# Kernel tuning notes

Hardware: AMD Instinct MI355X
Metric: run time of the kernel (lower is better)

The kernel has to match this reference:

```python
import jax, jax.numpy as jnp
import numpy as np

EMB = 64          # emb_size
LG = 64           # lg_msg_dim
NDB = 16          # num_dist_basis
NCB = 16          # num_cos_basis
NCLS = 40
NLAYERS = 2
NJK = NLAYERS + 2  # jumping-knowledge sequence length
HID = (NJK * EMB) // 2  # PyG JK-LSTM hidden size = 128


def setup_inputs() -> dict:
    key = jax.random.key(0)
    ks = jax.random.split(key, 24)
    N, Eg, Elg, F = 50000, 800000, 800000, 128
    s = 0.05
    inp = {
        "x": jax.random.normal(ks[0], (N, F), jnp.float32),
        "edge_index_g": jax.random.randint(ks[1], (2, Eg), 0, N, jnp.int32),
        "edge_attr_g": jax.random.uniform(ks[2], (Eg, NDB), jnp.float32),
        "edge_index_lg": jax.random.randint(ks[3], (2, Elg), 0, Eg, jnp.int32),
        "edge_attr_lg": jax.random.uniform(ks[4], (Elg, NCB), jnp.float32),
        # parameters (nn.Linear convention: W is [out, in])
        "W_feat": jax.random.normal(ks[5], (EMB, F), jnp.float32) * s,
        "W_msg": jax.random.normal(ks[6], (LG, 2 * EMB + NDB), jnp.float32) * s,
        "W_lg2g": jax.random.normal(ks[7], (EMB, LG), jnp.float32) * s,
        "b_lg2g": jax.random.normal(ks[8], (EMB,), jnp.float32) * s,
        "W_msg_layers": jax.random.normal(ks[9], (NLAYERS, LG, 2 * LG + NCB), jnp.float32) * s,
        # bidirectional LSTM params (PyTorch gate order i,f,g,o)
        "Wih_f": jax.random.normal(ks[10], (4 * HID, EMB), jnp.float32) * s,
        "Whh_f": jax.random.normal(ks[11], (4 * HID, HID), jnp.float32) * s,
        "bih_f": jax.random.normal(ks[12], (4 * HID,), jnp.float32) * s,
        "bhh_f": jax.random.normal(ks[13], (4 * HID,), jnp.float32) * s,
        "Wih_b": jax.random.normal(ks[14], (4 * HID, EMB), jnp.float32) * s,
        "Whh_b": jax.random.normal(ks[15], (4 * HID, HID), jnp.float32) * s,
        "bih_b": jax.random.normal(ks[16], (4 * HID,), jnp.float32) * s,
        "bhh_b": jax.random.normal(ks[17], (4 * HID,), jnp.float32) * s,
        "W_att": jax.random.normal(ks[18], (1, 2 * HID), jnp.float32) * s,
        "b_att": jax.random.normal(ks[19], (1,), jnp.float32) * s,
        "W_out": jax.random.normal(ks[20], (NCLS, EMB), jnp.float32) * s,
    }
    return inp


def _lstm(x_seq, Wih, Whh, bih, bhh, reverse):
    # x_seq: [N, L, C] -> hs: [N, L, H]
    N = x_seq.shape[0]
    H = Whh.shape[1]
    b = bih + bhh

    def step(carry, x_t):
        h, c = carry
        gates = x_t @ Wih.T + h @ Whh.T + b
        i, f, g, o = jnp.split(gates, 4, axis=-1)
        c = jax.nn.sigmoid(f) * c + jax.nn.sigmoid(i) * jnp.tanh(g)
        h = jax.nn.sigmoid(o) * jnp.tanh(c)
        return (h, c), h

    xs = jnp.swapaxes(x_seq, 0, 1)  # [L, N, C]
    init = (jnp.zeros((N, H), x_seq.dtype), jnp.zeros((N, H), x_seq.dtype))
    _, hs = jax.lax.scan(step, init, xs, reverse=reverse)
    return jnp.swapaxes(hs, 0, 1)


def reference(x, edge_index_g, edge_attr_g, edge_index_lg, edge_attr_lg,
              W_feat, W_msg, W_lg2g, b_lg2g, W_msg_layers,
              Wih_f, Whh_f, bih_f, bhh_f, Wih_b, Whh_b, bih_b, bhh_b,
              W_att, b_att, W_out):
    N = x.shape[0]
    Eg = edge_attr_g.shape[0]
    seg = jax.ops.segment_sum

    # node embedding (eval mode: dropout is identity)
    node_emb = jax.nn.relu(x @ W_feat.T)  # [N, EMB]

    # initial linegraph node features: gather endpoints -> concat -> linear -> relu
    m1 = node_emb[edge_index_g[0]]  # [Eg, EMB]
    m2 = node_emb[edge_index_g[1]]
    msg_emb = jax.nn.relu(jnp.concatenate([m1, m2, edge_attr_g], -1) @ W_msg.T)  # [Eg, LG]

    node_embs = [node_emb]
    msg_red = msg_emb @ W_lg2g.T + b_lg2g
    node_embs.append(seg(msg_red, edge_index_g[1], num_segments=N))

    # message-passing layers on the linegraph
    for l in range(W_msg_layers.shape[0]):
        s = msg_emb[edge_index_lg[0]]
        d = msg_emb[edge_index_lg[1]]
        m = jax.nn.relu(jnp.concatenate([s, d, edge_attr_lg], -1) @ W_msg_layers[l].T)
        msg_emb = seg(m, edge_index_lg[1], num_segments=Eg)  # scatter_add over linegraph
        incoming = seg(msg_emb, edge_index_g[1], num_segments=N)
        node_embs.append(incoming @ W_lg2g.T + b_lg2g)

    # JumpingKnowledge ('lstm'): bidirectional LSTM -> attention -> weighted sum
    x_jk = jnp.stack(node_embs, axis=1)  # [N, NJK, EMB]
    h_f = _lstm(x_jk, Wih_f, Whh_f, bih_f, bhh_f, reverse=False)
    h_b = _lstm(x_jk, Wih_b, Whh_b, bih_b, bhh_b, reverse=True)
    h = jnp.concatenate([h_f, h_b], -1)  # [N, NJK, 2*HID]
    alpha = jax.nn.softmax((h @ W_att.T + b_att)[..., 0], axis=-1)  # [N, NJK]
    final_emb = jnp.sum(x_jk * alpha[..., None], axis=1)  # [N, EMB]

    out = final_emb @ W_out.T
    return jax.nn.log_softmax(out, axis=-1)
```

## Files before the change

### kernel.cpp

```cpp
#include <hip/hip_runtime.h>

typedef unsigned short u16;
typedef unsigned int u32;
typedef __attribute__((ext_vector_type(8))) short bf16x8;
typedef __attribute__((ext_vector_type(4))) float f32x4;

#define MFMA(a, b, c) __builtin_amdgcn_mfma_f32_16x16x32_bf16(a, b, c, 0, 0, 0)

__device__ __forceinline__ u16 f2bf(float x) {
    union { float f; u32 u; } v; v.f = x;
    u32 r = (v.u + 0x7FFFu + ((v.u >> 16) & 1u)) >> 16;
    return (u16)r;
}
__device__ __forceinline__ float bf2f(u16 b) {
    union { u32 u; float f; } v; v.u = ((u32)b) << 16;
    return v.f;
}
__device__ __forceinline__ void casAddPair(u32* w, float lo, float hi) {
    u32 old = *w, assumed;
    do {
        assumed = old;
        u32 des = (u32)f2bf(bf2f((u16)(assumed & 0xFFFFu)) + lo) |
                  ((u32)f2bf(bf2f((u16)(assumed >> 16)) + hi) << 16);
        if (des == assumed) break;
        old = atomicCAS(w, assumed, des);
    } while (old != assumed);
}

__global__ __launch_bounds__(256) void prep_w(
    const float* __restrict__ Whh_f, const float* __restrict__ Whh_b,
    const float* __restrict__ Wih_f, const float* __restrict__ Wih_b,
    const float* __restrict__ bih_f, const float* __restrict__ bhh_f,
    const float* __restrict__ bih_b, const float* __restrict__ bhh_b,
    u16* __restrict__ WhhB, u16* __restrict__ WihB, float* __restrict__ BS)
{
    int i = blockIdx.x * 256 + threadIdx.x;
    if (i < 131072) {
        int d = i >> 16, r = i & 65535;
        WhhB[i] = f2bf(d ? Whh_b[r] : Whh_f[r]);
    } else if (i < 196608) {
        int i2 = i - 131072; int d = i2 >> 15, r = i2 & 32767;
        WihB[i2] = f2bf(d ? Wih_b[r] : Wih_f[r]);
    } else if (i < 197632) {
        int i3 = i - 196608; int d = i3 >> 9, g = i3 & 511;
        BS[i3] = d ? (bih_b[g] + bhh_b[g]) : (bih_f[g] + bhh_f[g]);
    }
}

__global__ __launch_bounds__(256) void count_kernel(const int* __restrict__ dst,
                                                    u32* __restrict__ cnt, long E)
{
    long i = (long)blockIdx.x * 256 + threadIdx.x;
    if (i < E) atomicAdd(&cnt[dst[i]], 1u);
}

__global__ __launch_bounds__(256) void scan1(const u32* __restrict__ a,
                                             u32* __restrict__ part, int n)
{
    __shared__ u32 ts[256];
    int b = blockIdx.x, t = threadIdx.x;
    long i0 = (long)b * 1024 + t * 4;
    u32 s = 0;
#pragma unroll
    for (int k = 0; k < 4; ++k) { long i = i0 + k; if (i < n) s += a[i]; }
    ts[t] = s; __syncthreads();
    for (int off = 1; off < 256; off <<= 1) {
        u32 x = (t >= off) ? ts[t - off] : 0u;
        __syncthreads(); ts[t] += x; __syncthreads();
    }
    if (t == 255) part[b] = ts[255];
}

__global__ __launch_bounds__(1024) void scan2(u32* __restrict__ part, int nb,
                                              u32* __restrict__ total_out)
{
    __shared__ u32 ts[1024];
    int t = threadIdx.x;
    u32 v = (t < nb) ? part[t] : 0u;
    ts[t] = v; __syncthreads();
    for (int off = 1; off < 1024; off <<= 1) {
        u32 x = (t >= off) ? ts[t - off] : 0u;
        __syncthreads(); ts[t] += x; __syncthreads();
    }
    if (t < nb) part[t] = ts[t] - v;
    if (t == 1023 && total_out) *total_out = ts[1023];
}

__global__ __launch_bounds__(256) void scan3(u32* __restrict__ a,
                                             const u32* __restrict__ part, int n)
{
    __shared__ u32 ts[256];
    int b = blockIdx.x, t = threadIdx.x;
    long i0 = (long)b * 1024 + t * 4;
    u32 v[4]; u32 s = 0;
#pragma unroll
    for (int k = 0; k < 4; ++k) { long i = i0 + k; v[k] = (i < n) ? a[i] : 0u; s += v[k]; }
    ts[t] = s; __syncthreads();
    for (int off = 1; off < 256; off <<= 1) {
        u32 x = (t >= off) ? ts[t - off] : 0u;
        __syncthreads(); ts[t] += x; __syncthreads();
    }
    u32 run = part[b] + ts[t] - s;
#pragma unroll
    for (int k = 0; k < 4; ++k) {
        long i = i0 + k;
        if (i < n) { u32 x = v[k]; a[i] = run; run += x; }
    }
}

__global__ __launch_bounds__(256) void fill_kernel(const int* __restrict__ dst,
                                                   u32* __restrict__ off,
                                                   int* __restrict__ list, long E)
{
    long i = (long)blockIdx.x * 256 + threadIdx.x;
    if (i < E) {
        u32 pos = atomicAdd(&off[dst[i]], 1u);
        list[pos] = (int)i;
    }
}

__global__ __launch_bounds__(256) void zero_fill(const u32* __restrict__ offc,
                                                 u16* __restrict__ outb, long NB)
{
    long idx = (long)blockIdx.x * 256 + threadIdx.x;
    long n = idx >> 3; int q = (int)(idx & 7);
    if (n >= NB) return;
    u32 s = n ? offc[n - 1] : 0u;
    u32 e = offc[n];
    bool need = (s == e) || ((s >> 7) != ((e - 1) >> 7));
    if (need) *(uint4*)(outb + n * 64 + q * 8) = make_uint4(0, 0, 0, 0);
}

template <int K, bool RELU, bool INBF16>
__global__ __launch_bounds__(256) void rowgemm(
    const void* __restrict__ in, const float* __restrict__ W,
    const float* __restrict__ bias, const float* __restrict__ bias_scale,
    u16* __restrict__ outb, int M)
{
    constexpr int KP = K + 8;
    __shared__ u16 inS[64 * KP];
    __shared__ u16 WS[64 * KP];
    int t = threadIdx.x;
    long rb = (long)blockIdx.x * 64;
    for (int i = t; i < 64 * K; i += 256) {
        int c = i / K, k = i - c * K;
        WS[c * KP + k] = f2bf(W[i]);
    }
    if (INBF16) {
        const u16* inb = (const u16*)in;
        for (int i = t; i < 64 * K / 8; i += 256) {
            int r = i / (K / 8), q = i - r * (K / 8);
            long gr = rb + r;
            uint4 v = make_uint4(0, 0, 0, 0);
            if (gr < M) v = *(const uint4*)&inb[gr * (long)K + q * 8];
            *(uint4*)&inS[r * KP + q * 8] = v;
        }
    } else {
        const float* inf = (const float*)in;
        for (int i = t; i < 64 * K; i += 256) {
            int r = i / K, k = i - r * K;
            long gr = rb + r;
            inS[r * KP + k] = (gr < M) ? f2bf(inf[gr * (long)K + k]) : (u16)0;
        }
    }
    __syncthreads();
    int l = t & 63, w = t >> 6, lr = l & 15, lq = l >> 4;
    f32x4 acc[4];
#pragma unroll
    for (int i = 0; i < 4; ++i) acc[i] = (f32x4){0.f, 0.f, 0.f, 0.f};
#pragma unroll
    for (int kc = 0; kc < K; kc += 32) {
        bf16x8 a = *(const bf16x8*)&inS[(w * 16 + lr) * KP + kc + lq * 8];
#pragma unroll
        for (int ct = 0; ct < 4; ++ct) {
            bf16x8 b = *(const bf16x8*)&WS[(ct * 16 + lr) * KP + kc + lq * 8];
            acc[ct] = MFMA(a, b, acc[ct]);
        }
    }
#pragma unroll
    for (int ct = 0; ct < 4; ++ct)
#pragma unroll
        for (int r = 0; r < 4; ++r) {
            long gr = rb + w * 16 + lq * 4 + r;
            if (gr < M) {
                int c = ct * 16 + lr;
                float v = acc[ct][r];
                if (bias) v += bias[c] * (bias_scale ? bias_scale[gr] : 1.f);
                if (RELU) v = fmaxf(v, 0.f);
                outb[gr * 64 + c] = f2bf(v);
            }
        }
}

__global__ __launch_bounds__(512, 4) void edge_msg_init2(
    const u16* __restrict__ feat, const int* __restrict__ ei,
    const float* __restrict__ attr, const float* __restrict__ W,
    u16* __restrict__ outb, long E)
{
    __shared__ u16 WS[64 * 168];
    __shared__ u16 eds[128 * 64];
    int t = threadIdx.x;
    long eb = (long)blockIdx.x * 128;
    for (int i = t; i < 64 * 144; i += 512) {
        int c = i / 144, k = i - c * 144;
        WS[c * 168 + k] = f2bf(W[i]);
    }
    for (int i = t; i < 64 * 24; i += 512) {
        int c = i / 24, k = 144 + (i - c * 24);
        WS[c * 168 + k] = 0;
    }
    int w = t >> 6, l = t & 63, lr = l & 15, lq = l >> 4;
    long e = eb + w * 16 + lr;
    long ec = (e < E) ? e : (E - 1);
    int src = ei[ec], dst = ei[E + ec];
    bf16x8 A[5];
    {
        const uint4* sp = (const uint4*)(feat + (long)src * 64);
        const uint4* dp = (const uint4*)(feat + (long)dst * 64);
        *(uint4*)&A[0] = sp[lq];
        *(uint4*)&A[1] = sp[4 + lq];
        *(uint4*)&A[2] = dp[lq];
        *(uint4*)&A[3] = dp[4 + lq];
        uint4 pv = make_uint4(0, 0, 0, 0);
        if (lq < 2) {
            const float4* ap = (const float4*)(attr + ec * 16) + lq * 2;
            float4 b0 = ap[0], b1 = ap[1];
            pv.x = (u32)f2bf(b0.x) | ((u32)f2bf(b0.y) << 16);
            pv.y = (u32)f2bf(b0.z) | ((u32)f2bf(b0.w) << 16);
            pv.z = (u32)f2bf(b1.x) | ((u32)f2bf(b1.y) << 16);
            pv.w = (u32)f2bf(b1.z) | ((u32)f2bf(b1.w) << 16);
        }
        *(uint4*)&A[4] = pv;
    }
    __syncthreads();
    f32x4 acc[4];
#pragma unroll
    for (int ct = 0; ct < 4; ++ct) acc[ct] = (f32x4){0.f, 0.f, 0.f, 0.f};
#pragma unroll
    for (int kc = 0; kc < 5; ++kc) {
#pragma unroll
        for (int ct = 0; ct < 4; ++ct) {
            bf16x8 b = *(const bf16x8*)&WS[(ct * 16 + lr) * 168 + kc * 32 + lq * 8];
            acc[ct] = MFMA(A[kc], b, acc[ct]);
        }
    }
#pragma unroll
    for (int ct = 0; ct < 4; ++ct)
#pragma unroll
        for (int r = 0; r < 4; ++r) {
            int row = w * 16 + lq * 4 + r;
            int col = ct * 16 + lr;
            eds[row * 64 + col] = f2bf(fmaxf(acc[ct][r], 0.f));
        }
    __syncthreads();
    for (int j = t; j < 1024; j += 512) {
        int le = j >> 3, q = j & 7;
        long e2 = eb + le;
        if (e2 < E)
            *(uint4*)(outb + e2 * 64 + q * 8) = *(const uint4*)&eds[le * 64 + q * 8];
    }
}

__global__ __launch_bounds__(512, 4) void edge_msg_lg2(
    const u16* __restrict__ feat, const int* __restrict__ ei,
    const float* __restrict__ attr, const float* __restrict__ W,
    const int* __restrict__ list, u16* __restrict__ outb, long E)
{
    __shared__ u16 WS[64 * 168];
    __shared__ u16 eds[128 * 64];
    __shared__ int dstS[128];
    __shared__ int idS[128];
    __shared__ int srcS[128];
    __shared__ int dprevS, dnextS;
    int t = threadIdx.x;
    long pb = (long)blockIdx.x * 128;
    for (int i = t; i < 64 * 144; i += 512) {
        int c = i / 144, k = i - c * 144;
        WS[c * 168 + k] = f2bf(W[i]);
    }
    for (int i = t; i < 64 * 24; i += 512) {
        int c = i / 24, k = 144 + (i - c * 24);
        WS[c * 168 + k] = 0;
    }
    if (t < 128) {
        long p = pb + t;
        int id = (p < E) ? list[p] : -1;
        idS[t] = id;
        srcS[t] = (id >= 0) ? ei[id] : 0;
        dstS[t] = (id >= 0) ? ei[E + id] : -1;
    } else if (t == 128) {
        dprevS = (pb > 0) ? ei[E + list[pb - 1]] : -2;
    } else if (t == 129) {
        dnextS = (pb + 128 < E) ? ei[E + list[pb + 128]] : -2;
    }
    __syncthreads();
    int w = t >> 6, l = t & 63, lr = l & 15, lq = l >> 4;
    int el = w * 16 + lr;
    int id = idS[el];
    long idc = (id >= 0) ? (long)id : 0;
    int src = srcS[el];
    int dst = (dstS[el] >= 0) ? dstS[el] : 0;
    bf16x8 A[5];
    {
        const uint4* sp = (const uint4*)(feat + (long)src * 64);
        const uint4* dp = (const uint4*)(feat + (long)dst * 64);
        *(uint4*)&A[0] = sp[lq];
        *(uint4*)&A[1] = sp[4 + lq];
        *(uint4*)&A[2] = dp[lq];
        *(uint4*)&A[3] = dp[4 + lq];
        uint4 pv = make_uint4(0, 0, 0, 0);
        if (lq < 2) {
            const float4* ap = (const float4*)(attr + idc * 16) + lq * 2;
            float4 b0 = ap[0], b1 = ap[1];
            pv.x = (u32)f2bf(b0.x) | ((u32)f2bf(b0.y) << 16);
            pv.y = (u32)f2bf(b0.z) | ((u32)f2bf(b0.w) << 16);
            pv.z = (u32)f2bf(b1.x) | ((u32)f2bf(b1.y) << 16);
            pv.w = (u32)f2bf(b1.z) | ((u32)f2bf(b1.w) << 16);
        }
        *(uint4*)&A[4] = pv;
    }
    f32x4 acc[4];
#pragma unroll
    for (int ct = 0; ct < 4; ++ct) acc[ct] = (f32x4){0.f, 0.f, 0.f, 0.f};
#pragma unroll
    for (int kc = 0; kc < 5; ++kc) {
#pragma unroll
        for (int ct = 0; ct < 4; ++ct) {
            bf16x8 b = *(const bf16x8*)&WS[(ct * 16 + lr) * 168 + kc * 32 + lq * 8];
            acc[ct] = MFMA(A[kc], b, acc[ct]);
        }
    }
#pragma unroll
    for (int ct = 0; ct < 4; ++ct)
#pragma unroll
        for (int r = 0; r < 4; ++r) {
            int row = w * 16 + lq * 4 + r;
            int col = ct * 16 + lr;
            eds[row * 64 + col] = f2bf(fmaxf(acc[ct][r], 0.f));
        }
    __syncthreads();
    for (int j = t; j < 4096; j += 512) {
        int le = j >> 5, wd = j & 31;
        int d = dstS[le];
        if (d < 0) continue;
        if (le > 0 && dstS[le - 1] == d) continue;
        float lo = 0.f, hi = 0.f;
        int le2 = le;
        do {
            u32 pair = *(const u32*)&eds[le2 * 64 + wd * 2];
            lo += bf2f((u16)(pair & 0xFFFFu));
            hi += bf2f((u16)(pair >> 16));
            ++le2;
        } while (le2 < 128 && dstS[le2] == d);
        bool bprev = (le == 0 && dprevS == d);
        bool bnext = (le2 == 128 && dnextS == d);
        u32* dw = (u32*)(outb + (long)d * 64 + wd * 2);
        if (bprev || bnext) {
            casAddPair(dw, lo, hi);
        } else {
            *dw = (u32)f2bf(lo) | ((u32)f2bf(hi) << 16);
        }
    }
}

__global__ __launch_bounds__(256) void gather_g(
    const u16* __restrict__ m, const int* __restrict__ list,
    const u32* __restrict__ offc, u16* __restrict__ aggB,
    float* __restrict__ degOut, int N)
{
    int t = threadIdx.x;
    int hw = t >> 5, c = t & 31;
    long n = (long)blockIdx.x * 8 + hw;
    if (n >= N) return;
    u32 start = n ? offc[n - 1] : 0u;
    u32 end = offc[n];
    float s0 = 0.f, s1 = 0.f;
    for (u32 i = start; i < end; ++i) {
        int e = list[i];
        u32 pair = *(const u32*)&m[(long)e * 64 + c * 2];
        s0 += bf2f((u16)(pair & 0xFFFFu));
        s1 += bf2f((u16)(pair >> 16));
    }
    *(u32*)&aggB[n * 64 + c * 2] = (u32)f2bf(s0) | ((u32)f2bf(s1) << 16);
    if (degOut && c == 0) degOut[n] = (float)(end - start);
}

__global__ __launch_bounds__(512, 2) void lstm3(
    const u16* __restrict__ jkB, const u16* __restrict__ WhhB,
    const u16* __restrict__ WihB, const float* __restrict__ BS,
    const float* __restrict__ Watt, float* __restrict__ scores,
    int N, int ntiles)
{
    __shared__ u16 hS[64 * 136];
    __shared__ u16 xS[64 * 72];
    __shared__ float WattS[128];
    __shared__ float part[64 * 8];
    int t = threadIdx.x;
    int dir = blockIdx.y;
    int w = t >> 6, l = t & 63, lr = l & 15, lq = l >> 4;
    const u16* WhhD = WhhB + (long)dir * 65536;
    const u16* WihD = WihB + (long)dir * 32768;
    int grow = w * 16 + lr;
    bf16x8 Wh[4][4], Wi[4][2];
    float bs[4];
#pragma unroll
    for (int ty = 0; ty < 4; ++ty) {
        int g = ty * 128 + grow;
#pragma unroll
        for (int kc = 0; kc < 4; ++kc)
            Wh[ty][kc] = *(const bf16x8*)&WhhD[g * 128 + kc * 32 + lq * 8];
#pragma unroll
        for (int kc = 0; kc < 2; ++kc)
            Wi[ty][kc] = *(const bf16x8*)&WihD[g * 64 + kc * 32 + lq * 8];
        bs[ty] = BS[dir * 512 + g];
    }
    if (t < 128) WattS[t] = Watt[dir * 128 + t];
    float* scOut = scores + (long)dir * N * 4;

    for (int tile = blockIdx.x; tile < ntiles; tile += gridDim.x) {
        long n0 = (long)tile * 64;
        __syncthreads();
        for (int i = t; i < 64 * 136; i += 512) hS[i] = 0;
        float creg[4][4] = {};
#pragma unroll 1
        for (int s = 0; s < 4; ++s) {
            int tt = dir ? (3 - s) : s;
            {
                int n = t >> 3, j = t & 7;
                long gn = n0 + n;
                uint4 v = make_uint4(0, 0, 0, 0);
                if (gn < N) v = *(const uint4*)&jkB[((long)tt * N + gn) * 64 + j * 8];
                *(uint4*)&xS[n * 72 + j * 8] = v;
            }
            __syncthreads();
            f32x4 acc[4][4];
#pragma unroll
            for (int ty = 0; ty < 4; ++ty)
#pragma unroll
                for (int nt = 0; nt < 4; ++nt) {
                    float b0 = bs[ty];
                    acc[ty][nt] = (f32x4){b0, b0, b0, b0};
                }
#pragma unroll
            for (int kc = 0; kc < 4; ++kc) {
                bf16x8 a[4];
#pragma unroll
                for (int nt = 0; nt < 4; ++nt)
                    a[nt] = *(const bf16x8*)&hS[(nt * 16 + lr) * 136 + kc * 32 + lq * 8];
#pragma unroll
                for (int ty = 0; ty < 4; ++ty)
#pragma unroll
                    for (int nt = 0; nt < 4; ++nt)
                        acc[ty][nt] = MFMA(a[nt], Wh[ty][kc], acc[ty][nt]);
            }
#pragma unroll
            for (int kc = 0; kc < 2; ++kc) {
                bf16x8 a[4];
#pragma unroll
                for (int nt = 0; nt < 4; ++nt)
                    a[nt] = *(const bf16x8*)&xS[(nt * 16 + lr) * 72 + kc * 32 + lq * 8];
#pragma unroll
                for (int ty = 0; ty < 4; ++ty)
#pragma unroll
                    for (int nt = 0; nt < 4; ++nt)
                        acc[ty][nt] = MFMA(a[nt], Wi[ty][kc], acc[ty][nt]);
            }
            __syncthreads();
#pragma unroll
            for (int nt = 0; nt < 4; ++nt)
#pragma unroll
                for (int r = 0; r < 4; ++r) {
                    float iv = acc[0][nt][r], fv = acc[1][nt][r];
                    float gv = acc[2][nt][r], ov = acc[3][nt][r];
                    float c = creg[nt][r];
                    float si = 1.f / (1.f + __expf(-iv));
                    float sf = 1.f / (1.f + __expf(-fv));
                    float tg = 2.f / (1.f + __expf(-2.f * gv)) - 1.f;
                    c = sf * c + si * tg;
                    float so = 1.f / (1.f + __expf(-ov));
                    float th = 2.f / (1.f + __expf(-2.f * c)) - 1.f;
                    creg[nt][r] = c;
                    int node = nt * 16 + lq * 4 + r;
                    hS[node * 136 + grow] = f2bf(so * th);
                }
            __syncthreads();
            {
                int n = t & 63, ck = t >> 6;
                float sum = 0.f;
#pragma unroll
                for (int j = 0; j < 16; ++j)
                    sum += bf2f(hS[n * 136 + ck * 16 + j]) * WattS[ck * 16 + j];
                part[n * 8 + ck] = sum;
            }
            __syncthreads();
            if (t < 64) {
                long gn = n0 + t;
                if (gn < N) {
                    float v = 0.f;
#pragma unroll
                    for (int j = 0; j < 8; ++j) v += part[t * 8 + j];
                    scOut[gn * 4 + tt] = v;
                }
            }
        }
    }
}

__global__ __launch_bounds__(256) void final_kernel(
    const u16* __restrict__ jkB, const float* __restrict__ scores,
    const float* __restrict__ Wout, float* __restrict__ out, int N)
{
    __shared__ float feS[4][64];
    int t = threadIdx.x, l = t & 63, w = t >> 6;
    long n = (long)blockIdx.x * 4 + w;
    bool ok = (n < N);
    long nn = ok ? n : (long)(N - 1);
    float sc[4];
#pragma unroll
    for (int tt = 0; tt < 4; ++tt)
        sc[tt] = scores[nn * 4 + tt] + scores[(long)N * 4 + nn * 4 + tt];
    float m = fmaxf(fmaxf(sc[0], sc[1]), fmaxf(sc[2], sc[3]));
    float e0 = __expf(sc[0] - m), e1 = __expf(sc[1] - m);
    float e2 = __expf(sc[2] - m), e3 = __expf(sc[3] - m);
    float den = e0 + e1 + e2 + e3;
    float a0 = e0 / den, a1 = e1 / den, a2 = e2 / den, a3 = e3 / den;
    float fe = a0 * bf2f(jkB[nn * 64 + l]) + a1 * bf2f(jkB[((long)N + nn) * 64 + l]) +
               a2 * bf2f(jkB[((long)2 * N + nn) * 64 + l]) +
               a3 * bf2f(jkB[((long)3 * N + nn) * 64 + l]);
    feS[w][l] = fe;
    __syncthreads();
    float logit = 0.f;
    if (l < 40)
        for (int c = 0; c < 64; ++c) logit += feS[w][c] * Wout[l * 64 + c];
    float v = (l < 40) ? logit : -1e30f;
    for (int off = 32; off; off >>= 1) v = fmaxf(v, __shfl_xor(v, off));
    float ex = (l < 40) ? __expf(logit - v) : 0.f;
    for (int off = 32; off; off >>= 1) ex += __shfl_xor(ex, off);
    if (ok && l < 40) out[n * 40 + l] = logit - v - __logf(ex);
}

extern "C" void kernel_launch(void* const* d_in, const int* in_sizes, int n_in,
                              void* d_out, int out_size, void* d_ws, size_t ws_size,
                              hipStream_t stream)
{
    const float* x        = (const float*)d_in[0];
    const int*   eig      = (const int*)d_in[1];
    const float* eag      = (const float*)d_in[2];
    const int*   eilg     = (const int*)d_in[3];
    const float* ealg     = (const float*)d_in[4];
    const float* W_feat   = (const float*)d_in[5];
    const float* W_msg    = (const float*)d_in[6];
    const float* W_lg2g   = (const float*)d_in[7];
    const float* b_lg2g   = (const float*)d_in[8];
    const float* W_msg_l  = (const float*)d_in[9];
    const float* Wih_f    = (const float*)d_in[10];
    const float* Whh_f    = (const float*)d_in[11];
    const float* bih_f    = (const float*)d_in[12];
    const float* bhh_f    = (const float*)d_in[13];
    const float* Wih_b    = (const float*)d_in[14];
    const float* Whh_b    = (const float*)d_in[15];
    const float* bih_b    = (const float*)d_in[16];
    const float* bhh_b    = (const float*)d_in[17];
    const float* W_att    = (const float*)d_in[18];
    const float* W_out    = (const float*)d_in[20];

    int  N   = in_sizes[0] / 128;
    long Eg  = in_sizes[1] / 2;
    long Elg = in_sizes[3] / 2;

    char* wp = (char*)d_ws;
    auto alloc = [&](size_t bytes) -> char* {
        char* p = wp; wp += (bytes + 255) & ~(size_t)255; return p;
    };
    u16*   jkB    = (u16*)  alloc((size_t)4 * N * 64 * 2);
    u16*   mA     = (u16*)  alloc((size_t)Eg * 64 * 2);
    u16*   mB     = (u16*)  alloc((size_t)Eg * 64 * 2);
    u16*   aggB   = (u16*)  alloc((size_t)N * 64 * 2);
    float* deg    = (float*)alloc((size_t)N * 4);
    float* scores = (float*)alloc((size_t)2 * N * 4 * 4);
    u16*   WhhB   = (u16*)  alloc((size_t)2 * 65536 * 2);
    u16*   WihB   = (u16*)  alloc((size_t)2 * 32768 * 2);
    float* BS     = (float*)alloc((size_t)2 * 512 * 4);
    u32*   off_g  = (u32*)  alloc((size_t)(N + 1) * 4);
    int*   list_g = (int*)  alloc((size_t)Eg * 4);
    u32*   off_lg = (u32*)  alloc((size_t)(Eg + 1) * 4);
    int*   list_lg= (int*)  alloc((size_t)Elg * 4);
    u32*   part   = (u32*)  alloc((size_t)1024 * 4);

    prep_w<<<772, 256, 0, stream>>>(Whh_f, Whh_b, Wih_f, Wih_b,
                                    bih_f, bhh_f, bih_b, bhh_b, WhhB, WihB, BS);
    hipMemsetAsync(off_g, 0, (size_t)(N + 1) * 4, stream);
    count_kernel<<<(int)((Eg + 255) / 256), 256, 0, stream>>>(eig + Eg, off_g, Eg);
    {
        int nb = (N + 1023) / 1024;
        scan1<<<nb, 256, 0, stream>>>(off_g, part, N);
        scan2<<<1, 1024, 0, stream>>>(part, nb, off_g + N);
        scan3<<<nb, 256, 0, stream>>>(off_g, part, N);
    }
    fill_kernel<<<(int)((Eg + 255) / 256), 256, 0, stream>>>(eig + Eg, off_g, list_g, Eg);
    hipMemsetAsync(off_lg, 0, (size_t)(Eg + 1) * 4, stream);
    count_kernel<<<(int)((Elg + 255) / 256), 256, 0, stream>>>(eilg + Elg, off_lg, Elg);
    {
        int nb = (int)((Eg + 1023) / 1024);
        scan1<<<nb, 256, 0, stream>>>(off_lg, part, (int)Eg);
        scan2<<<1, 1024, 0, stream>>>(part, nb, off_lg + Eg);
        scan3<<<nb, 256, 0, stream>>>(off_lg, part, (int)Eg);
    }
    fill_kernel<<<(int)((Elg + 255) / 256), 256, 0, stream>>>(eilg + Elg, off_lg, list_lg, Elg);

    rowgemm<128, true, false><<<(N + 63) / 64, 256, 0, stream>>>(
        x, W_feat, nullptr, nullptr, jkB, N);
    edge_msg_init2<<<(int)((Eg + 127) / 128), 512, 0, stream>>>(
        jkB, eig, eag, W_msg, mA, Eg);
    gather_g<<<(N + 7) / 8, 256, 0, stream>>>(mA, list_g, off_g, aggB, deg, N);
    rowgemm<64, false, true><<<(N + 63) / 64, 256, 0, stream>>>(
        aggB, W_lg2g, b_lg2g, deg, jkB + (size_t)N * 64, N);
    zero_fill<<<(int)((Eg * 8 + 255) / 256), 256, 0, stream>>>(off_lg, mB, Eg);
    edge_msg_lg2<<<(int)((Elg + 127) / 128), 512, 0, stream>>>(
        mA, eilg, ealg, W_msg_l, list_lg, mB, Elg);
    gather_g<<<(N + 7) / 8, 256, 0, stream>>>(mB, list_g, off_g, aggB, nullptr, N);
    rowgemm<64, false, true><<<(N + 63) / 64, 256, 0, stream>>>(
        aggB, W_lg2g, b_lg2g, nullptr, jkB + (size_t)2 * N * 64, N);
    zero_fill<<<(int)((Eg * 8 + 255) / 256), 256, 0, stream>>>(off_lg, mA, Eg);
    edge_msg_lg2<<<(int)((Elg + 127) / 128), 512, 0, stream>>>(
        mB, eilg, ealg, W_msg_l + 64 * 144, list_lg, mA, Elg);
    gather_g<<<(N + 7) / 8, 256, 0, stream>>>(mA, list_g, off_g, aggB, nullptr, N);
    rowgemm<64, false, true><<<(N + 63) / 64, 256, 0, stream>>>(
        aggB, W_lg2g, b_lg2g, nullptr, jkB + (size_t)3 * N * 64, N);
    {
        int ntiles = (N + 63) / 64;
        lstm3<<<dim3(512, 2), 512, 0, stream>>>(
            jkB, WhhB, WihB, BS, W_att, scores, N, ntiles);
    }
    final_kernel<<<(N + 3) / 4, 256, 0, stream>>>(
        jkB, scores, W_out, (float*)d_out, N);
}
```

Before: 1.136 ms.

## Restructure JK-LSTM kernel: one tile per block, preload inputs, fused attention reduce

The LSTM kernel now launches one block per 64-node tile instead of a persistent grid loop, and preloads all four timestep inputs into shared memory up front. The log2(e) scaling is folded into the weights and biases at prep time so the gates use raw exp2 and rcp intrinsics. The MFMA operands are swapped so each lane holds four consecutive gate rows, which lets the attention dot product be done in registers with shuffles. The first step's recurrent GEMM is skipped because h is zero, and several barriers are removed. The trade-off is more shared memory per block, reloading weights in every block, and slightly lower precision in the approximate transcendentals.

```diff
diff --git a/kernel.cpp b/kernel.cpp
--- a/kernel.cpp
+++ b/kernel.cpp
@@ -34,16 +34,20 @@
     const float* __restrict__ bih_b, const float* __restrict__ bhh_b,
     u16* __restrict__ WhhB, u16* __restrict__ WihB, float* __restrict__ BS)
 {
+    const float L2E = 1.4426950408889634f;
     int i = blockIdx.x * 256 + threadIdx.x;
     if (i < 131072) {
         int d = i >> 16, r = i & 65535;
-        WhhB[i] = f2bf(d ? Whh_b[r] : Whh_f[r]);
+        float s = (((r >> 14) & 3) == 2) ? 2.f * L2E : L2E;
+        WhhB[i] = f2bf(s * (d ? Whh_b[r] : Whh_f[r]));
     } else if (i < 196608) {
         int i2 = i - 131072; int d = i2 >> 15, r = i2 & 32767;
-        WihB[i2] = f2bf(d ? Wih_b[r] : Wih_f[r]);
+        float s = (((r >> 13) & 3) == 2) ? 2.f * L2E : L2E;
+        WihB[i2] = f2bf(s * (d ? Wih_b[r] : Wih_f[r]));
     } else if (i < 197632) {
         int i3 = i - 196608; int d = i3 >> 9, g = i3 & 511;
-        BS[i3] = d ? (bih_b[g] + bhh_b[g]) : (bih_f[g] + bhh_f[g]);
+        float s = (((g >> 7) & 3) == 2) ? 2.f * L2E : L2E;
+        BS[i3] = s * (d ? (bih_b[g] + bhh_b[g]) : (bih_f[g] + bhh_f[g]));
     }
 }
 
@@ -389,58 +393,60 @@
     const u16* __restrict__ jkB, const u16* __restrict__ WhhB,
     const u16* __restrict__ WihB, const float* __restrict__ BS,
     const float* __restrict__ Watt, float* __restrict__ scores,
-    int N, int ntiles)
+    int N)
 {
     __shared__ u16 hS[64 * 136];
-    __shared__ u16 xS[64 * 72];
-    __shared__ float WattS[128];
-    __shared__ float part[64 * 8];
+    __shared__ u16 xS[4][64 * 72];
+    __shared__ float part[4 * 64 * 8];
     int t = threadIdx.x;
     int dir = blockIdx.y;
     int w = t >> 6, l = t & 63, lr = l & 15, lq = l >> 4;
     const u16* WhhD = WhhB + (long)dir * 65536;
     const u16* WihD = WihB + (long)dir * 32768;
-    int grow = w * 16 + lr;
+    long n0 = (long)blockIdx.x * 64;
+
+    {
+        int n = t >> 3, j = t & 7;
+        long gn = n0 + n;
+#pragma unroll
+        for (int k = 0; k < 4; ++k) {
+            uint4 v = make_uint4(0, 0, 0, 0);
+            if (gn < N) v = *(const uint4*)&jkB[((long)k * N + gn) * 64 + j * 8];
+            *(uint4*)&xS[k][n * 72 + j * 8] = v;
+        }
+    }
+
+    int grow0 = w * 16 + lq * 4;
     bf16x8 Wh[4][4], Wi[4][2];
-    float bs[4];
+    float4 b4[4];
 #pragma unroll
     for (int ty = 0; ty < 4; ++ty) {
-        int g = ty * 128 + grow;
+        int g = ty * 128 + w * 16 + lr;
 #pragma unroll
         for (int kc = 0; kc < 4; ++kc)
             Wh[ty][kc] = *(const bf16x8*)&WhhD[g * 128 + kc * 32 + lq * 8];
 #pragma unroll
         for (int kc = 0; kc < 2; ++kc)
             Wi[ty][kc] = *(const bf16x8*)&WihD[g * 64 + kc * 32 + lq * 8];
-        bs[ty] = BS[dir * 512 + g];
-    }
-    if (t < 128) WattS[t] = Watt[dir * 128 + t];
+        b4[ty] = *(const float4*)&BS[dir * 512 + ty * 128 + grow0];
+    }
+    float4 Wa4 = *(const float4*)&Watt[dir * 128 + grow0];
     float* scOut = scores + (long)dir * N * 4;
 
-    for (int tile = blockIdx.x; tile < ntiles; tile += gridDim.x) {
-        long n0 = (long)tile * 64;
-        __syncthreads();
-        for (int i = t; i < 64 * 136; i += 512) hS[i] = 0;
-        float creg[4][4] = {};
+    float creg[4][4] = {};
+    __syncthreads();
+
 #pragma unroll 1
-        for (int s = 0; s < 4; ++s) {
-            int tt = dir ? (3 - s) : s;
-            {
-                int n = t >> 3, j = t & 7;
-                long gn = n0 + n;
-                uint4 v = make_uint4(0, 0, 0, 0);
-                if (gn < N) v = *(const uint4*)&jkB[((long)tt * N + gn) * 64 + j * 8];
-                *(uint4*)&xS[n * 72 + j * 8] = v;
-            }
-            __syncthreads();
-            f32x4 acc[4][4];
-#pragma unroll
-            for (int ty = 0; ty < 4; ++ty)
-#pragma unroll
-                for (int nt = 0; nt < 4; ++nt) {
-                    float b0 = bs[ty];
-                    acc[ty][nt] = (f32x4){b0, b0, b0, b0};
-                }
+    for (int s = 0; s < 4; ++s) {
+        int tt = dir ? (3 - s) : s;
+        f32x4 acc[4][4];
+#pragma unroll
+        for (int ty = 0; ty < 4; ++ty) {
+            f32x4 bv = {b4[ty].x, b4[ty].y, b4[ty].z, b4[ty].w};
+#pragma unroll
+            for (int nt = 0; nt < 4; ++nt) acc[ty][nt] = bv;
+        }
+        if (s) {
 #pragma unroll
             for (int kc = 0; kc < 4; ++kc) {
                 bf16x8 a[4];
@@ -451,57 +457,60 @@
                 for (int ty = 0; ty < 4; ++ty)
 #pragma unroll
                     for (int nt = 0; nt < 4; ++nt)
-                        acc[ty][nt] = MFMA(a[nt], Wh[ty][kc], acc[ty][nt]);
+                        acc[ty][nt] = MFMA(Wh[ty][kc], a[nt], acc[ty][nt]);
             }
-#pragma unroll
-            for (int kc = 0; kc < 2; ++kc) {
-                bf16x8 a[4];
+        }
+#pragma unroll
+        for (int kc = 0; kc < 2; ++kc) {
+            bf16x8 a[4];
+#pragma unroll
+            for (int nt = 0; nt < 4; ++nt)
+                a[nt] = *(const bf16x8*)&xS[tt][(nt * 16 + lr) * 72 + kc * 32 + lq * 8];
+#pragma unroll
+            for (int ty = 0; ty < 4; ++ty)
 #pragma unroll
                 for (int nt = 0; nt < 4; ++nt)
-                    a[nt] = *(const bf16x8*)&xS[(nt * 16 + lr) * 72 + kc * 32 + lq * 8];
-#pragma unroll
-                for (int ty = 0; ty < 4; ++ty)
-#pragma unroll
-                    for (int nt = 0; nt < 4; ++nt)
-                        acc[ty][nt] = MFMA(a[nt], Wi[ty][kc], acc[ty][nt]);
+                    acc[ty][nt] = MFMA(Wi[ty][kc], a[nt], acc[ty][nt]);
+        }
+        if (s) __syncthreads();
+#pragma unroll
+        for (int nt = 0; nt < 4; ++nt) {
+            float hv[4];
+#pragma unroll
+            for (int r = 0; r < 4; ++r) {
+                float iv = acc[0][nt][r], fv = acc[1][nt][r];
+                float gv = acc[2][nt][r], ov = acc[3][nt][r];
+                float c = creg[nt][r];
+                float si = __builtin_amdgcn_rcpf(1.f + __builtin_amdgcn_exp2f(-iv));
+                float sf = __builtin_amdgcn_rcpf(1.f + __builtin_amdgcn_exp2f(-fv));
+                float tg = 2.f * __builtin_amdgcn_rcpf(1.f + __builtin_amdgcn_exp2f(-gv)) - 1.f;
+                c = sf * c + si * tg;
+                float so = __builtin_amdgcn_rcpf(1.f + __builtin_amdgcn_exp2f(-ov));
+                float th = 2.f * __builtin_amdgcn_rcpf(
+                               1.f + __builtin_amdgcn_exp2f(-2.8853900817779268f * c)) - 1.f;
+                creg[nt][r] = c;
+                hv[r] = so * th;
             }
-            __syncthreads();
-#pragma unroll
-            for (int nt = 0; nt < 4; ++nt)
-#pragma unroll
-                for (int r = 0; r < 4; ++r) {
-                    float iv = acc[0][nt][r], fv = acc[1][nt][r];
-                    float gv = acc[2][nt][r], ov = acc[3][nt][r];
-                    float c = creg[nt][r];
-                    float si = 1.f / (1.f + __expf(-iv));
-                    float sf = 1.f / (1.f + __expf(-fv));
-                    float tg = 2.f / (1.f + __expf(-2.f * gv)) - 1.f;
-                    c = sf * c + si * tg;
-                    float so = 1.f / (1.f + __expf(-ov));
-                    float th = 2.f / (1.f + __expf(-2.f * c)) - 1.f;
-                    creg[nt][r] = c;
-                    int node = nt * 16 + lq * 4 + r;
-                    hS[node * 136 + grow] = f2bf(so * th);
-                }
-            __syncthreads();
-            {
-                int n = t & 63, ck = t >> 6;
-                float sum = 0.f;
-#pragma unroll
-                for (int j = 0; j < 16; ++j)
-                    sum += bf2f(hS[n * 136 + ck * 16 + j]) * WattS[ck * 16 + j];
-                part[n * 8 + ck] = sum;
+            float p = hv[0] * Wa4.x + hv[1] * Wa4.y + hv[2] * Wa4.z + hv[3] * Wa4.w;
+            p += __shfl_xor(p, 16);
+            p += __shfl_xor(p, 32);
+            if (lq == 0) part[(tt * 64 + nt * 16 + lr) * 8 + w] = p;
+            if (s < 3) {
+                u32 p0 = (u32)f2bf(hv[0]) | ((u32)f2bf(hv[1]) << 16);
+                u32 p1 = (u32)f2bf(hv[2]) | ((u32)f2bf(hv[3]) << 16);
+                *(uint2*)&hS[(nt * 16 + lr) * 136 + grow0] = make_uint2(p0, p1);
             }
-            __syncthreads();
-            if (t < 64) {
-                long gn = n0 + t;
-                if (gn < N) {
-                    float v = 0.f;
-#pragma unroll
-                    for (int j = 0; j < 8; ++j) v += part[t * 8 + j];
-                    scOut[gn * 4 + tt] = v;
-                }
-            }
+        }
+        if (s < 3) __syncthreads();
+    }
+    __syncthreads();
+    if (t < 256) {
+        int tt = t >> 6, node = t & 63;
+        long gn = n0 + node;
+        if (gn < N) {
+            const float4* pp = (const float4*)&part[(tt * 64 + node) * 8];
+            float4 a = pp[0], b = pp[1];
+            scOut[gn * 4 + tt] = a.x + a.y + a.z + a.w + b.x + b.y + b.z + b.w;
         }
     }
 }
@@ -629,8 +638,8 @@
         aggB, W_lg2g, b_lg2g, nullptr, jkB + (size_t)3 * N * 64, N);
     {
         int ntiles = (N + 63) / 64;
-        lstm3<<<dim3(512, 2), 512, 0, stream>>>(
-            jkB, WhhB, WihB, BS, W_att, scores, N, ntiles);
+        lstm3<<<dim3(ntiles, 2), 512, 0, stream>>>(
+            jkB, WhhB, WihB, BS, W_att, scores, N);
     }
     final_kernel<<<(N + 3) / 4, 256, 0, stream>>>(
         jkB, scores, W_out, (float*)d_out, N);
```

Result: faster. 1.103 ms (-2.9%).
